# Optimization experiments

Measured on AMD Instinct MI355X. Metric: run time of the kernel, lower is better.

Reference implementation:

```python
import jax, jax.numpy as jnp
import numpy as np

N = 200000   # active voxels
C = 64       # channels (INIT_DIM / PLANES[0])
K = 27       # 3^3 kernel offsets for 3D kernel_size=3
M = 100000   # gather/scatter pairs per kernel offset
EPS = 1e-5


def setup_inputs() -> dict:
    key = jax.random.key(0)
    ks = jax.random.split(key, 8)
    x = jax.random.normal(ks[0], (N, C), jnp.float32)
    # kaiming-ish scale for sparse conv kernels [K, Cin, Cout]
    scale = 1.0 / np.sqrt(K * C)
    w1 = jax.random.normal(ks[1], (K, C, C), jnp.float32) * scale
    w2 = jax.random.normal(ks[2], (K, C, C), jnp.float32) * scale
    in_map = jax.random.randint(ks[3], (K, M), 0, N, dtype=jnp.int32)
    out_map = jax.random.randint(ks[4], (K, M), 0, N, dtype=jnp.int32)
    gamma1 = jnp.ones((C,), jnp.float32)
    beta1 = jnp.zeros((C,), jnp.float32)
    mean1 = jax.random.normal(ks[5], (C,), jnp.float32) * 0.1
    var1 = jax.random.uniform(ks[6], (C,), jnp.float32) + 0.5
    gamma2 = jnp.ones((C,), jnp.float32)
    beta2 = jnp.zeros((C,), jnp.float32)
    mean2 = jax.random.normal(ks[7], (C,), jnp.float32) * 0.1
    var2 = jax.random.uniform(jax.random.fold_in(key, 7), (C,), jnp.float32) + 0.5
    return dict(x=x, w1=w1, w2=w2,
                gamma1=gamma1, beta1=beta1, mean1=mean1, var1=var1,
                gamma2=gamma2, beta2=beta2, mean2=mean2, var2=var2,
                in_map=in_map, out_map=out_map)


def sparse_conv(x, w, in_map, out_map):
    """Gather-GEMM-scatter sparse convolution (MinkowskiConvolution core).
    x: [N, Cin]; w: [K, Cin, Cout]; in_map/out_map: [K, M] voxel indices.
    """
    g = x[in_map]                                  # [K, M, Cin] gather
    y = jnp.einsum('kmc,kcd->kmd', g, w)           # per-offset GEMM
    cout = w.shape[-1]
    out = jnp.zeros((N, cout), x.dtype)
    out = out.at[out_map.reshape(-1)].add(y.reshape(-1, cout))  # scatter-add
    return out


def batch_norm(x, gamma, beta, mean, var):
    return (x - mean) * jax.lax.rsqrt(var + EPS) * gamma + beta


def reference(x, w1, w2, gamma1, beta1, mean1, var1,
              gamma2, beta2, mean2, var2, in_map, out_map):
    # BasicBlock: conv1 -> BN -> ReLU -> conv2 -> BN -> +residual -> ReLU
    out = sparse_conv(x, w1, in_map, out_map)
    out = jax.nn.relu(batch_norm(out, gamma1, beta1, mean1, var1))
    out = sparse_conv(out, w2, in_map, out_map)
    out = batch_norm(out, gamma2, beta2, mean2, var2)
    return jax.nn.relu(out + x)
```

## Files before the change

kernel.cpp:

```cpp
#include <hip/hip_runtime.h>
#include <stdint.h>

#define N_VOX    200000
#define C_CH     64
#define K_OFF    27
#define M_PAIRS  100000
#define KM       (K_OFF * M_PAIRS)
#define TILE     64
#define NT       (N_VOX / TILE)
#define NB       (NT * K_OFF)
#define WBN      (K_OFF * 4096)
#define EPS_BN   1e-5f
#define CDCAP    (KM / 16 + NB + 64)

#define SLICES   16
#define SLICE_LEN (M_PAIRS / SLICES)
#define KB       (K_OFF * SLICES)
#define PTS      3200

#define SCHUNK   2048
#define NBLK1    ((NB + SCHUNK - 1) / SCHUNK)
#define PQ1      0
#define PQ2      128

#define YCAP     1040
#define CLCAP    160

typedef __attribute__((ext_vector_type(8))) short   short8_t;
typedef __attribute__((ext_vector_type(4))) float   f32x4;

__device__ __forceinline__ unsigned short f2bf(float f) {
    union { float f; unsigned u; } v; v.f = f;
    unsigned r = v.u + 0x7FFFu + ((v.u >> 16) & 1u);
    return (unsigned short)(r >> 16);
}
__device__ __forceinline__ float bf2f(unsigned u16) {
    union { unsigned u; float f; } v; v.u = u16 << 16;
    return v.f;
}
__device__ __forceinline__ int pmap(int cs) {
    int p = cs >> 1, h = cs & 1;
    return (p & 3) * 16 + (p >> 2) * 2 + h;
}

__global__ void prep_kernel(const float* __restrict__ x,
                            const float* __restrict__ w1, const float* __restrict__ w2,
                            const float* __restrict__ g1, const float* __restrict__ b1,
                            const float* __restrict__ m1, const float* __restrict__ v1,
                            const float* __restrict__ g2, const float* __restrict__ b2,
                            const float* __restrict__ m2, const float* __restrict__ v2,
                            unsigned short* __restrict__ xb,
                            unsigned short* __restrict__ wb1, unsigned short* __restrict__ wb2,
                            float* __restrict__ sbp1, float* __restrict__ sbp2)
{
    long i = (long)blockIdx.x * blockDim.x + threadIdx.x;
    const long XBN8 = (long)N_VOX * C_CH / 8;
    if (i < XBN8) {
        const f32x4* sp = (const f32x4*)(x + (size_t)i * 8);
        f32x4 a = sp[0], b = sp[1];
        uint4 o;
        o.x = (unsigned)f2bf(a[0]) | ((unsigned)f2bf(a[1]) << 16);
        o.y = (unsigned)f2bf(a[2]) | ((unsigned)f2bf(a[3]) << 16);
        o.z = (unsigned)f2bf(b[0]) | ((unsigned)f2bf(b[1]) << 16);
        o.w = (unsigned)f2bf(b[2]) | ((unsigned)f2bf(b[3]) << 16);
        ((uint4*)xb)[i] = o;
        return;
    }
    long j = i - XBN8;
    if (j < 2 * WBN) {
        int isw2 = j >= WBN;
        int o = (int)(isw2 ? j - WBN : j);
        int k   = o >> 12;
        int rem = o & 4095;
        int t  = rem >> 11;
        int sl = (rem >> 9) & 3;
        int d  = (rem >> 3) & 63;
        int jj = rem & 7;
        int cs = t * 32 + sl * 8 + jj;
        if (!isw2) wb1[o] = f2bf(w1[k * 4096 + cs * 64 + d]);
        else       wb2[o] = f2bf(w2[k * 4096 + pmap(cs) * 64 + d]);
        return;
    }
    j -= 2 * WBN;
    if (j < 128) {
        int L = (int)(j >= 64);
        int ch = (int)(j & 63);
        float gv = L ? g2[ch] : g1[ch];
        float vv = L ? v2[ch] : v1[ch];
        float mv = L ? m2[ch] : m1[ch];
        float bv = L ? b2[ch] : b1[ch];
        float s = gv * rsqrtf(vv + EPS_BN);
        float sh = bv - mv * s;
        int n = ch >> 4, rem = ch & 15, m = rem >> 1, h = rem & 1;
        int idx = 2 * (m * 4 + n) + h;
        float* sbp = L ? sbp2 : sbp1;
        sbp[idx] = s; sbp[64 + idx] = sh;
    }
}

__global__ __launch_bounds__(256) void hist_kernel(const int* __restrict__ out_map,
                                                   int* __restrict__ partial)
{
    __shared__ int h[3136];
    int blk = blockIdx.x;
    int k = blk >> 4, s = blk & 15;
    int tid = threadIdx.x;
    for (int i = tid; i < 3136; i += 256) h[i] = 0;
    __syncthreads();
    int p0 = k * M_PAIRS + s * SLICE_LEN;
    for (int i = tid; i < SLICE_LEN; i += 256)
        atomicAdd(&h[out_map[p0 + i] >> 6], 1);
    __syncthreads();
    for (int t = tid; t < NT; t += 256)
        partial[blk * PTS + t] = h[t];
}

__global__ __launch_bounds__(256) void transp_kernel(const int* __restrict__ partial,
                                                     int* __restrict__ partial_T)
{
    __shared__ int tb[32][33];
    int bx = blockIdx.x % 14, by = blockIdx.x / 14;
    int kb0 = bx * 32, t0 = by * 32;
    int tx = threadIdx.x & 31, ty = threadIdx.x >> 5;
    #pragma unroll
    for (int dy = 0; dy < 32; dy += 8) {
        int kb = kb0 + ty + dy;
        tb[ty + dy][tx] = (kb < KB) ? partial[kb * PTS + t0 + tx] : 0;
    }
    __syncthreads();
    #pragma unroll
    for (int dy = 0; dy < 32; dy += 8) {
        int t = t0 + ty + dy;
        int kb = kb0 + tx;
        if (t < NT && kb < KB)
            partial_T[t * KB + kb] = tb[tx][ty + dy];
    }
}

__global__ __launch_bounds__(256) void scanA_kernel(const int* __restrict__ partial_T,
                                                    int* __restrict__ part)
{
    __shared__ int lds[256], lds2[256];
    int b0 = blockIdx.x * SCHUNK;
    int t = threadIdx.x;
    int sraw = 0, sc16 = 0;
    for (int i = t; i < SCHUNK; i += 256) {
        int b = b0 + i;
        if (b < NB) {
            int tt = b / K_OFF, k = b % K_OFF;
            const int* pr = &partial_T[tt * KB + k * SLICES];
            int c = 0;
            #pragma unroll
            for (int s = 0; s < SLICES; ++s) c += pr[s];
            sraw += c; sc16 += (c + 15) >> 4;
        }
    }
    lds[t] = sraw; lds2[t] = sc16;
    __syncthreads();
    for (int d = 128; d > 0; d >>= 1) {
        if (t < d) { lds[t] += lds[t + d]; lds2[t] += lds2[t + d]; }
        __syncthreads();
    }
    if (t == 0) { part[PQ1 + blockIdx.x] = lds[0]; part[PQ2 + blockIdx.x] = lds2[0]; }
}

__global__ __launch_bounds__(128) void scanB_kernel(int* __restrict__ part) {
    __shared__ int lds[128];
    int g = blockIdx.x, t = threadIdx.x;
    int base = (g == 0) ? PQ1 : PQ2;
    int v = (t < NBLK1) ? part[base + t] : 0;
    lds[t] = v;
    __syncthreads();
    for (int d = 1; d < 128; d <<= 1) {
        int u = (t >= d) ? lds[t - d] : 0;
        __syncthreads();
        lds[t] += u;
        __syncthreads();
    }
    if (t < NBLK1) part[base + t] = lds[t] - v;
}

__global__ __launch_bounds__(256) void scanC_kernel(const int* __restrict__ partial_T,
                                                    const int* __restrict__ part,
                                                    int* __restrict__ offs,
                                                    int* __restrict__ cdoffs,
                                                    int* __restrict__ base)
{
    __shared__ int lds[256], lds2[256];
    int b = blockIdx.x, t = threadIdx.x;
    int i0 = b * SCHUNK + t * 8;
    int c[8]; int sraw = 0, sc16 = 0;
    #pragma unroll
    for (int j = 0; j < 8; ++j) {
        int idx = i0 + j;
        int tot = 0;
        if (idx < NB) {
            int tt = idx / K_OFF, k = idx - tt * K_OFF;
            const int* pr = &partial_T[tt * KB + k * SLICES];
            #pragma unroll
            for (int s = 0; s < SLICES; ++s) tot += pr[s];
        }
        c[j] = tot;
        sraw += tot; sc16 += (tot + 15) >> 4;
    }
    int vr = sraw, vc = sc16;
    lds[t] = vr; lds2[t] = vc;
    __syncthreads();
    for (int d = 1; d < 256; d <<= 1) {
        int ur = (t >= d) ? lds[t - d] : 0;
        int uc = (t >= d) ? lds2[t - d] : 0;
        __syncthreads();
        lds[t] += ur; lds2[t] += uc;
        __syncthreads();
    }
    int braw = part[PQ1 + b] + lds[t] - vr;
    int bc16 = part[PQ2 + b] + lds2[t] - vc;
    #pragma unroll
    for (int j = 0; j < 8; ++j) {
        int idx = i0 + j;
        if (idx < NB) {
            offs[idx] = braw; cdoffs[idx] = bc16;
            int tt = idx / K_OFF, k = idx - tt * K_OFF;
            const int* pr = &partial_T[tt * KB + k * SLICES];
            int run = braw;
            #pragma unroll
            for (int s = 0; s < SLICES; ++s) {
                base[(k * SLICES + s) * PTS + tt] = run;
                run += pr[s];
            }
        }
        braw += c[j]; bc16 += (c[j] + 15) >> 4;
    }
    if (b == NBLK1 - 1 && t == 255) { offs[NB] = braw; cdoffs[NB] = bc16; }
}

__global__ __launch_bounds__(256) void scatter2_kernel(const int* __restrict__ in_map,
                                                       const int* __restrict__ out_map,
                                                       const int* __restrict__ base,
                                                       unsigned* __restrict__ pp)
{
    __shared__ int lbase[NT];
    __shared__ int h2[NT];
    int blk = blockIdx.x;
    int k = blk >> 4, s = blk & 15;
    int tid = threadIdx.x;
    const int* gb = &base[(k * SLICES + s) * PTS];
    for (int i = tid; i < NT; i += 256) { lbase[i] = gb[i]; h2[i] = 0; }
    __syncthreads();
    int p0 = k * M_PAIRS + s * SLICE_LEN;
    #pragma unroll 2
    for (int i = tid; i < SLICE_LEN; i += 256) {
        int p = p0 + i;
        int o = out_map[p];
        int t = o >> 6;
        int rank = atomicAdd(&h2[t], 1);
        pp[lbase[t] + rank] = (unsigned)in_map[p] | ((unsigned)(o & 63) << 18);
    }
}

__global__ void cdescb_kernel(const int* __restrict__ offs, const int* __restrict__ cdoffs,
                              unsigned long long* __restrict__ cdesc)
{
    int b = blockIdx.x * 256 + threadIdx.x;
    if (b >= NB) return;
    int k = b % K_OFF;
    int c0 = cdoffs[b];
    int nchunk = cdoffs[b + 1] - c0;
    int base = offs[b];
    int end  = offs[b + 1];
    for (int i = 0; i < nchunk; ++i)
        cdesc[c0 + i] = (unsigned long long)k
                      | ((unsigned long long)(base + 16 * i) << 5)
                      | ((unsigned long long)end << 27);
}

template<int LAYER>
__global__ __launch_bounds__(1024, 1) void fused_kernel(
    const unsigned short* __restrict__ xin,
    const unsigned short* __restrict__ wb,
    const unsigned* __restrict__ pp,
    const unsigned long long* __restrict__ cdesc,
    const int* __restrict__ offs,
    const int* __restrict__ cdoffs,
    const float* __restrict__ sbp,
    const float* __restrict__ xres,
    void* __restrict__ outp)
{
    __shared__ unsigned Ylds[(YCAP + 8) * 32];
    __shared__ unsigned ppl[YCAP];
    __shared__ unsigned long long cl[CLCAP];
    __shared__ unsigned short ridx[YCAP];
    __shared__ unsigned short rrank[YCAP];
    __shared__ unsigned char  soloc[YCAP];
    __shared__ int hist[TILE];
    __shared__ int cstart[TILE + 1];

    const int tile = blockIdx.x;
    const int tid = threadIdx.x;
    const int p0 = offs[tile * K_OFF];
    const int p1 = offs[(tile + 1) * K_OFF];
    const int c0 = cdoffs[tile * K_OFF];
    const int c1 = cdoffs[(tile + 1) * K_OFF];
    const int nch = c1 - c0;
    int nr = p1 - p0; if (nr > YCAP) nr = YCAP;

    for (int i = tid; i < nch && i < CLCAP; i += 1024) cl[i] = cdesc[c0 + i];
    if (tid < TILE) hist[tid] = 0;
    __syncthreads();
    for (int i = tid; i < nr; i += 1024) {
        unsigned pv = pp[p0 + i];
        ppl[i] = pv;
        int ol = (int)((pv >> 18) & 63);
        soloc[i] = (unsigned char)ol;
        rrank[i] = (unsigned short)atomicAdd(&hist[ol], 1);
    }
    __syncthreads();
    if (tid < 64) {
        int v = hist[tid];
        int s = v;
        #pragma unroll
        for (int d = 1; d < 64; d <<= 1) {
            int u = __shfl_up(s, d, 64);
            if (tid >= d) s += u;
        }
        cstart[tid] = s - v;
        if (tid == 63) cstart[64] = s;
    }
    __syncthreads();
    for (int i = tid; i < nr; i += 1024)
        ridx[cstart[soloc[i]] + rrank[i]] = (unsigned short)i;

    const int wid   = tid >> 6;
    const int lane  = tid & 63;
    const int r     = lane & 15;
    const int sfour = lane >> 4;
    const int par   = lane & 1;

    const int CPW = (nch + 15) >> 4;
    int w0 = wid * CPW; if (w0 > nch) w0 = nch;
    int w1 = w0 + CPW;  if (w1 > nch) w1 = nch;

    short8_t A0s[2], A1s[2];
    int yrs[2], kks[2];
    short8_t B0[4], B1[4];
    int kcur = -1;

#define ISSUE(S, CI) do {                                                     \
        int _ci = (CI);                                                       \
        if (_ci < w1) {                                                       \
            unsigned long long _d = (_ci < CLCAP) ? cl[_ci] : cdesc[c0 + _ci];\
            kks[S] = (int)(_d & 31);                                          \
            int _pbr = (int)((_d >> 5) & 0x3FFFFF) - p0;                      \
            int _per = (int)(_d >> 27) - p0;                                  \
            int _ii = _pbr + r;                                               \
            bool _real = _ii < _per;                                          \
            int _idx = _real ? _ii : _pbr;                                    \
            if (_idx >= YCAP) _idx = 0;                                       \
            unsigned _pv = ppl[_idx];                                         \
            yrs[S] = (_real && _ii < YCAP) ? _ii : (YCAP + (_ci & 7));        \
            const short8_t* _xr =                                             \
                (const short8_t*)(xin + (size_t)(_pv & 0x3FFFFu) * 64);       \
            A0s[S] = _xr[sfour];                                              \
            A1s[S] = _xr[4 + sfour];                                          \
        }                                                                     \
    } while (0)

#define CONSUME(S) do {                                                       \
        int _kk = kks[S];                                                     \
        if (_kk != kcur) {                                                    \
            kcur = _kk;                                                       \
            const short8_t* _wbk = (const short8_t*)(wb + kcur * 4096);       \
            _Pragma("unroll")                                                 \
            for (int n = 0; n < 4; ++n) {                                     \
                B0[n] = _wbk[sfour * 64 + n * 16 + r];                        \
                B1[n] = _wbk[(4 + sfour) * 64 + n * 16 + r];                  \
            }                                                                 \
        }                                                                     \
        f32x4 acc[4] = {{0,0,0,0},{0,0,0,0},{0,0,0,0},{0,0,0,0}};             \
        _Pragma("unroll")                                                     \
        for (int n = 0; n < 4; ++n) {                                         \
            acc[n] = __builtin_amdgcn_mfma_f32_16x16x32_bf16(A0s[S], B0[n], acc[n], 0, 0, 0); \
            acc[n] = __builtin_amdgcn_mfma_f32_16x16x32_bf16(A1s[S], B1[n], acc[n], 0, 0, 0); \
        }                                                                     \
        int _yr = yrs[S];                                                     \
        _Pragma("unroll")                                                     \
        for (int jj = 0; jj < 4; jj += 2) {                                   \
            uint4 _w;                                                         \
            unsigned* _wp = (unsigned*)&_w;                                   \
            _Pragma("unroll")                                                 \
            for (int n = 0; n < 4; ++n) {                                     \
                float _mine = par ? acc[n][jj + 1] : acc[n][jj];              \
                float _send = par ? acc[n][jj]     : acc[n][jj + 1];          \
                float _t = __shfl_xor(_send, 1, 64);                          \
                float _lo = par ? _t : _mine;                                 \
                float _hi = par ? _mine : _t;                                 \
                unsigned _pk;                                                 \
                asm("v_cvt_pk_bf16_f32 %0, %1, %2" : "=v"(_pk) : "v"(_lo), "v"(_hi)); \
                _wp[n] = _pk;                                                 \
            }                                                                 \
            int _Rw = sfour * 4 + jj + par;                                   \
            int _yrow = __shfl(_yr, _Rw, 64);                                 \
            *(uint4*)&Ylds[(unsigned)_yrow * 32 + (r >> 1) * 4] = _w;         \
        }                                                                     \
    } while (0)

    ISSUE(0, w0);
    ISSUE(1, w0 + 1);
    #pragma unroll 1
    for (int i = w0; i < w1; i += 2) {
        CONSUME(0); ISSUE(0, i + 2);
        if (i + 1 < w1) { CONSUME(1); ISSUE(1, i + 3); }
    }
#undef ISSUE
#undef CONSUME
    __syncthreads();

    const int v  = tid >> 4;
    const int q2 = tid & 15;
    int cs0 = cstart[v], cs1 = cstart[v + 1];
    float sum[4] = {0.f, 0.f, 0.f, 0.f};
    for (int j = cs0; j < cs1; ++j) {
        int row = (int)ridx[j];
        uint2 u = *(const uint2*)&Ylds[(unsigned)row * 32 + 2 * q2];
        sum[0] += bf2f(u.x & 0xFFFFu);
        sum[1] += bf2f(u.x >> 16);
        sum[2] += bf2f(u.y & 0xFFFFu);
        sum[3] += bf2f(u.y >> 16);
    }

    const int og = tile * TILE + v;
    const float2* sc2 = (const float2*)sbp;
    const float2* sh2 = (const float2*)(sbp + 64);
    int pA = 2 * q2, pB = 2 * q2 + 1;
    float a0 = sum[0] * sc2[pA].x + sh2[pA].x;
    float a1 = sum[1] * sc2[pA].y + sh2[pA].y;
    float b0 = sum[2] * sc2[pB].x + sh2[pB].x;
    float b1 = sum[3] * sc2[pB].y + sh2[pB].y;
    if (LAYER == 0) {
        a0 = a0 > 0.f ? a0 : 0.f; a1 = a1 > 0.f ? a1 : 0.f;
        b0 = b0 > 0.f ? b0 : 0.f; b1 = b1 > 0.f ? b1 : 0.f;
        uint2 o2;
        o2.x = (unsigned)f2bf(a0) | ((unsigned)f2bf(a1) << 16);
        o2.y = (unsigned)f2bf(b0) | ((unsigned)f2bf(b1) << 16);
        *(uint2*)((unsigned*)outp + (size_t)og * 32 + 2 * q2) = o2;
    } else {
        float* out = (float*)outp;
        int chA = (pA & 3) * 16 + (pA >> 2) * 2;
        int chB = (pB & 3) * 16 + (pB >> 2) * 2;
        float2 xrA = *(const float2*)(xres + (size_t)og * 64 + chA);
        float2 xrB = *(const float2*)(xres + (size_t)og * 64 + chB);
        a0 += xrA.x; a1 += xrA.y; b0 += xrB.x; b1 += xrB.y;
        a0 = a0 > 0.f ? a0 : 0.f; a1 = a1 > 0.f ? a1 : 0.f;
        b0 = b0 > 0.f ? b0 : 0.f; b1 = b1 > 0.f ? b1 : 0.f;
        *(float2*)(out + (size_t)og * 64 + chA) = make_float2(a0, a1);
        *(float2*)(out + (size_t)og * 64 + chB) = make_float2(b0, b1);
    }
}

extern "C" void kernel_launch(void* const* d_in, const int* in_sizes, int n_in,
                              void* d_out, int out_size, void* d_ws, size_t ws_size,
                              hipStream_t stream)
{
    const float* x  = (const float*)d_in[0];
    const float* w1 = (const float*)d_in[1];
    const float* w2 = (const float*)d_in[2];
    const float* g1 = (const float*)d_in[3];
    const float* b1 = (const float*)d_in[4];
    const float* m1 = (const float*)d_in[5];
    const float* v1 = (const float*)d_in[6];
    const float* g2 = (const float*)d_in[7];
    const float* b2 = (const float*)d_in[8];
    const float* m2 = (const float*)d_in[9];
    const float* v2 = (const float*)d_in[10];
    const int* in_map  = (const int*)d_in[11];
    const int* out_map = (const int*)d_in[12];

    char* ws = (char*)d_ws;
    size_t off = 0;
    auto alloc = [&](size_t bytes) -> void* {
        void* p = ws + off;
        off = (off + bytes + 255) & ~(size_t)255;
        return p;
    };
    int* partial   = (int*)alloc((size_t)KB * PTS * 4);
    int* partial_T = (int*)alloc((size_t)NT * KB * 4);
    int* base      = (int*)alloc((size_t)KB * PTS * 4);
    int* offs      = (int*)alloc((size_t)(NB + 1) * 4);
    int* cdoffs    = (int*)alloc((size_t)(NB + 1) * 4);
    int* part      = (int*)alloc(512 * 4);
    float* sbp1    = (float*)alloc(128 * 4);
    float* sbp2    = (float*)alloc(128 * 4);
    unsigned short* wb1 = (unsigned short*)alloc((size_t)WBN * 2);
    unsigned short* wb2 = (unsigned short*)alloc((size_t)WBN * 2);
    unsigned* pp   = (unsigned*)alloc((size_t)KM * 4);
    unsigned long long* cdesc = (unsigned long long*)alloc((size_t)CDCAP * 8);
    unsigned short* xb = (unsigned short*)alloc((size_t)N_VOX * C_CH * 2);
    unsigned short* hb = (unsigned short*)alloc((size_t)N_VOX * C_CH * 2);

    const long TOT = (long)N_VOX * C_CH / 8 + 2 * WBN + 128;
    prep_kernel<<<(int)((TOT + 255) / 256), 256, 0, stream>>>(
        x, w1, w2, g1, b1, m1, v1, g2, b2, m2, v2,
        xb, wb1, wb2, sbp1, sbp2);

    hist_kernel<<<KB, 256, 0, stream>>>(out_map, partial);
    transp_kernel<<<14 * ((NT + 31) / 32), 256, 0, stream>>>(partial, partial_T);
    scanA_kernel<<<NBLK1, 256, 0, stream>>>(partial_T, part);
    scanB_kernel<<<2, 128, 0, stream>>>(part);
    scanC_kernel<<<NBLK1, 256, 0, stream>>>(partial_T, part, offs, cdoffs, base);
    scatter2_kernel<<<KB, 256, 0, stream>>>(in_map, out_map, base, pp);
    cdescb_kernel<<<(NB + 255) / 256, 256, 0, stream>>>(offs, cdoffs, cdesc);

    fused_kernel<0><<<NT, 1024, 0, stream>>>(xb, wb1, pp, cdesc, offs, cdoffs,
                                             sbp1, nullptr, hb);
    fused_kernel<1><<<NT, 1024, 0, stream>>>(hb, wb2, pp, cdesc, offs, cdoffs,
                                             sbp2, x, d_out);
}
```

Before: 397.6 us.

## Halve output tile to 32 voxels and drop single-block occupancy bound

Shrinks the per-block output tile from 64 to 32 voxels. The histogram, partition, LDS buffers and pair-encoding bit widths shrink to match, and each thread now reduces one packed channel pair instead of two. The launch bound no longer forces one block per CU, so the smaller LDS footprint can let two 1024-thread blocks share a CU and twice as many blocks run. The cost is more blocks with more per-block setup overhead, and the 16 waves have less GEMM work to split per tile.

```diff
diff --git a/kernel.cpp b/kernel.cpp
--- a/kernel.cpp
+++ b/kernel.cpp
@@ -6,7 +6,7 @@
 #define K_OFF    27
 #define M_PAIRS  100000
 #define KM       (K_OFF * M_PAIRS)
-#define TILE     64
+#define TILE     32
 #define NT       (N_VOX / TILE)
 #define NB       (NT * K_OFF)
 #define WBN      (K_OFF * 4096)
@@ -16,15 +16,15 @@
 #define SLICES   16
 #define SLICE_LEN (M_PAIRS / SLICES)
 #define KB       (K_OFF * SLICES)
-#define PTS      3200
+#define PTS      6400
 
 #define SCHUNK   2048
 #define NBLK1    ((NB + SCHUNK - 1) / SCHUNK)
 #define PQ1      0
 #define PQ2      128
 
-#define YCAP     1040
-#define CLCAP    160
+#define YCAP     560
+#define CLCAP    112
 
 typedef __attribute__((ext_vector_type(8))) short   short8_t;
 typedef __attribute__((ext_vector_type(4))) float   f32x4;
@@ -101,15 +101,15 @@
 __global__ __launch_bounds__(256) void hist_kernel(const int* __restrict__ out_map,
                                                    int* __restrict__ partial)
 {
-    __shared__ int h[3136];
+    __shared__ int h[NT];
     int blk = blockIdx.x;
     int k = blk >> 4, s = blk & 15;
     int tid = threadIdx.x;
-    for (int i = tid; i < 3136; i += 256) h[i] = 0;
+    for (int i = tid; i < NT; i += 256) h[i] = 0;
     __syncthreads();
     int p0 = k * M_PAIRS + s * SLICE_LEN;
     for (int i = tid; i < SLICE_LEN; i += 256)
-        atomicAdd(&h[out_map[p0 + i] >> 6], 1);
+        atomicAdd(&h[out_map[p0 + i] >> 5], 1);
     __syncthreads();
     for (int t = tid; t < NT; t += 256)
         partial[blk * PTS + t] = h[t];
@@ -252,9 +252,9 @@
     for (int i = tid; i < SLICE_LEN; i += 256) {
         int p = p0 + i;
         int o = out_map[p];
-        int t = o >> 6;
+        int t = o >> 5;
         int rank = atomicAdd(&h2[t], 1);
-        pp[lbase[t] + rank] = (unsigned)in_map[p] | ((unsigned)(o & 63) << 18);
+        pp[lbase[t] + rank] = (unsigned)in_map[p] | ((unsigned)(o & 31) << 18);
     }
 }
 
@@ -275,7 +275,7 @@
 }
 
 template<int LAYER>
-__global__ __launch_bounds__(1024, 1) void fused_kernel(
+__global__ __launch_bounds__(1024) void fused_kernel(
     const unsigned short* __restrict__ xin,
     const unsigned short* __restrict__ wb,
     const unsigned* __restrict__ pp,
@@ -307,24 +307,26 @@
     for (int i = tid; i < nch && i < CLCAP; i += 1024) cl[i] = cdesc[c0 + i];
     if (tid < TILE) hist[tid] = 0;
     __syncthreads();
-    for (int i = tid; i < nr; i += 1024) {
-        unsigned pv = pp[p0 + i];
-        ppl[i] = pv;
-        int ol = (int)((pv >> 18) & 63);
-        soloc[i] = (unsigned char)ol;
-        rrank[i] = (unsigned short)atomicAdd(&hist[ol], 1);
-    }
-    __syncthreads();
-    if (tid < 64) {
+    if (tid < 1024) {
+        for (int i = tid; i < nr; i += 1024) {
+            unsigned pv = pp[p0 + i];
+            ppl[i] = pv;
+            int ol = (int)((pv >> 18) & 31);
+            soloc[i] = (unsigned char)ol;
+            rrank[i] = (unsigned short)atomicAdd(&hist[ol], 1);
+        }
+    }
+    __syncthreads();
+    if (tid < 32) {
         int v = hist[tid];
         int s = v;
         #pragma unroll
-        for (int d = 1; d < 64; d <<= 1) {
-            int u = __shfl_up(s, d, 64);
+        for (int d = 1; d < 32; d <<= 1) {
+            int u = __shfl_up(s, d, 32);
             if (tid >= d) s += u;
         }
         cstart[tid] = s - v;
-        if (tid == 63) cstart[64] = s;
+        if (tid == 31) cstart[32] = s;
     }
     __syncthreads();
     for (int i = tid; i < nr; i += 1024)
@@ -415,45 +417,35 @@
 #undef CONSUME
     __syncthreads();
 
-    const int v  = tid >> 4;
-    const int q2 = tid & 15;
+    const int v = tid >> 5;
+    const int q = tid & 31;
     int cs0 = cstart[v], cs1 = cstart[v + 1];
-    float sum[4] = {0.f, 0.f, 0.f, 0.f};
+    float s0 = 0.f, s1 = 0.f;
     for (int j = cs0; j < cs1; ++j) {
         int row = (int)ridx[j];
-        uint2 u = *(const uint2*)&Ylds[(unsigned)row * 32 + 2 * q2];
-        sum[0] += bf2f(u.x & 0xFFFFu);
-        sum[1] += bf2f(u.x >> 16);
-        sum[2] += bf2f(u.y & 0xFFFFu);
-        sum[3] += bf2f(u.y >> 16);
+        unsigned u = Ylds[(unsigned)row * 32 + q];
+        s0 += bf2f(u & 0xFFFFu);
+        s1 += bf2f(u >> 16);
     }
 
     const int og = tile * TILE + v;
     const float2* sc2 = (const float2*)sbp;
     const float2* sh2 = (const float2*)(sbp + 64);
-    int pA = 2 * q2, pB = 2 * q2 + 1;
-    float a0 = sum[0] * sc2[pA].x + sh2[pA].x;
-    float a1 = sum[1] * sc2[pA].y + sh2[pA].y;
-    float b0 = sum[2] * sc2[pB].x + sh2[pB].x;
-    float b1 = sum[3] * sc2[pB].y + sh2[pB].y;
+    float a0 = s0 * sc2[q].x + sh2[q].x;
+    float a1 = s1 * sc2[q].y + sh2[q].y;
     if (LAYER == 0) {
-        a0 = a0 > 0.f ? a0 : 0.f; a1 = a1 > 0.f ? a1 : 0.f;
-        b0 = b0 > 0.f ? b0 : 0.f; b1 = b1 > 0.f ? b1 : 0.f;
-        uint2 o2;
-        o2.x = (unsigned)f2bf(a0) | ((unsigned)f2bf(a1) << 16);
-        o2.y = (unsigned)f2bf(b0) | ((unsigned)f2bf(b1) << 16);
-        *(uint2*)((unsigned*)outp + (size_t)og * 32 + 2 * q2) = o2;
+        a0 = a0 > 0.f ? a0 : 0.f;
+        a1 = a1 > 0.f ? a1 : 0.f;
+        ((unsigned*)outp)[(size_t)og * 32 + q] =
+            (unsigned)f2bf(a0) | ((unsigned)f2bf(a1) << 16);
     } else {
         float* out = (float*)outp;
-        int chA = (pA & 3) * 16 + (pA >> 2) * 2;
-        int chB = (pB & 3) * 16 + (pB >> 2) * 2;
-        float2 xrA = *(const float2*)(xres + (size_t)og * 64 + chA);
-        float2 xrB = *(const float2*)(xres + (size_t)og * 64 + chB);
-        a0 += xrA.x; a1 += xrA.y; b0 += xrB.x; b1 += xrB.y;
-        a0 = a0 > 0.f ? a0 : 0.f; a1 = a1 > 0.f ? a1 : 0.f;
-        b0 = b0 > 0.f ? b0 : 0.f; b1 = b1 > 0.f ? b1 : 0.f;
-        *(float2*)(out + (size_t)og * 64 + chA) = make_float2(a0, a1);
-        *(float2*)(out + (size_t)og * 64 + chB) = make_float2(b0, b1);
+        int ch = (q & 3) * 16 + (q >> 2) * 2;
+        float2 xr = *(const float2*)(xres + (size_t)og * 64 + ch);
+        a0 += xr.x; a1 += xr.y;
+        a0 = a0 > 0.f ? a0 : 0.f;
+        a1 = a1 > 0.f ? a1 : 0.f;
+        *(float2*)(out + (size_t)og * 64 + ch) = make_float2(a0, a1);
     }
 }
 
```

Measured after the change: 513.0 us. 1.29x slower.
